# Optimization experiments

Measured on AMD Instinct MI355X. Metric: run time of the kernel, lower is better.

## Reference

```python
import jax, jax.numpy as jnp
import numpy as np

N_NODES = 100000
N_EDGES = 3200000
N_GRAPHS = 2048
DIM = 32
FEAT = 78
OUT = 128
BN_EPS = 1e-5


def setup_inputs() -> dict:
    key = jax.random.key(0)
    ks = jax.random.split(key, 16)
    x = jax.random.normal(ks[0], (N_NODES, FEAT), dtype=jnp.float32)
    edge_index = jax.random.randint(ks[1], (2, N_EDGES), 0, N_NODES, dtype=jnp.int64)
    batch = jnp.sort(jax.random.randint(ks[2], (N_NODES,), 0, N_GRAPHS, dtype=jnp.int64))
    s = 0.1
    # layer 1 MLP (78 -> 32 -> 32)
    W1a = jax.random.normal(ks[3], (FEAT, DIM), dtype=jnp.float32) * s
    b1a = jnp.zeros((DIM,), jnp.float32)
    W1b = jax.random.normal(ks[4], (DIM, DIM), dtype=jnp.float32) * s
    b1b = jnp.zeros((DIM,), jnp.float32)
    # layers 2-5 MLPs stacked (32 -> 32 -> 32)
    Wa = jax.random.normal(ks[5], (4, DIM, DIM), dtype=jnp.float32) * s
    ba = jnp.zeros((4, DIM), jnp.float32)
    Wb = jax.random.normal(ks[6], (4, DIM, DIM), dtype=jnp.float32) * s
    bb = jnp.zeros((4, DIM), jnp.float32)
    # batchnorm affine params for 5 layers
    gamma = jnp.ones((5, DIM), jnp.float32)
    beta = jnp.zeros((5, DIM), jnp.float32)
    # final graph-level linear 32 -> 128
    Wfc = jax.random.normal(ks[7], (DIM, OUT), dtype=jnp.float32) * s
    bfc = jnp.zeros((OUT,), jnp.float32)
    return {"x": x, "edge_index": edge_index, "batch": batch,
            "W1a": W1a, "b1a": b1a, "W1b": W1b, "b1b": b1b,
            "Wa": Wa, "ba": ba, "Wb": Wb, "bb": bb,
            "gamma": gamma, "beta": beta, "Wfc": Wfc, "bfc": bfc}


def _gin_layer(h, edge_index, Wa, ba, Wb, bb, g, b):
    # GIN aggregation (eps=0): h_i + sum_{j->i} h_j via scatter-add on dst
    src, dst = edge_index[0], edge_index[1]
    agg = h + jax.ops.segment_sum(h[src], dst, num_segments=h.shape[0])
    # tiny MLP: Linear -> ReLU -> Linear
    h = jax.nn.relu(agg @ Wa + ba) @ Wb + bb
    h = jax.nn.relu(h)
    # BatchNorm1d (training mode, biased variance)
    mu = h.mean(axis=0)
    var = ((h - mu) ** 2).mean(axis=0)
    return (h - mu) * jax.lax.rsqrt(var + BN_EPS) * g + b


def reference(x, edge_index, batch, W1a, b1a, W1b, b1b, Wa, ba, Wb, bb, gamma, beta, Wfc, bfc):
    h = _gin_layer(x, edge_index, W1a, b1a, W1b, b1b, gamma[0], beta[0])
    for i in range(4):
        h = _gin_layer(h, edge_index, Wa[i], ba[i], Wb[i], bb[i], gamma[i + 1], beta[i + 1])
    # global_add_pool over graphs
    pooled = jax.ops.segment_sum(h, batch, num_segments=N_GRAPHS)  # [G, 32]
    out = jax.nn.relu(pooled @ Wfc + bfc)  # dropout = identity in eval
    return out
```

## Files before the change

kernel.cpp:

```cpp
#include <hip/hip_runtime.h>
#include <hip/hip_fp16.h>

#define N_NODES 100000
#define N_GRAPHS 2048
#define N_EDGES 3200000
#define NHALF 50000
#define DIM 32
#define FEAT 78
#define OUT_DIM 128
#define BN_EPS 1e-5f

#define BSHIFT 9
#define BSIZE 512
#define NB ((N_NODES + BSIZE - 1) / BSIZE)
#define CHUNK 8192
#define NSUB 4

#define NTILES (N_NODES / 16)
#define SBINS 64
#define AGG_BLOCKS 3128

typedef _Float16 f16x8 __attribute__((ext_vector_type(8)));
typedef float f32x4 __attribute__((ext_vector_type(4)));

__global__ __launch_bounds__(256) void bucket_hist_kernel(const int* __restrict__ dst,
                                                          int* __restrict__ bcnt) {
    __shared__ int lh[256];
    int tid = threadIdx.x;
    lh[tid] = 0;
    __syncthreads();
    const int4* d4 = (const int4*)dst;
    const int n4 = N_EDGES / 4;
    int i = blockIdx.x * blockDim.x + tid;
    int stride = gridDim.x * blockDim.x;
    for (; i < n4; i += stride) {
        int4 v = d4[i];
        atomicAdd(&lh[v.x >> BSHIFT], 1);
        atomicAdd(&lh[v.y >> BSHIFT], 1);
        atomicAdd(&lh[v.z >> BSHIFT], 1);
        atomicAdd(&lh[v.w >> BSHIFT], 1);
    }
    __syncthreads();
    if (tid < NB && lh[tid])
        atomicAdd(&bcnt[tid], lh[tid]);
}

__global__ __launch_bounds__(256) void bucket_scan_kernel(const int* __restrict__ bcnt,
                                                          int* __restrict__ bstart,
                                                          int* __restrict__ bcursor,
                                                          int* __restrict__ rowst) {
    __shared__ int sc[256];
    int tid = threadIdx.x;
    int v = (tid < NB) ? bcnt[tid] : 0;
    sc[tid] = v;
    __syncthreads();
    for (int off = 1; off < 256; off <<= 1) {
        int nv = (tid >= off) ? sc[tid - off] : 0;
        __syncthreads();
        sc[tid] += nv;
        __syncthreads();
    }
    if (tid < NB) {
        int ex = sc[tid] - v;
        bstart[tid] = ex;
        bcursor[tid] = ex;
    }
    if (tid == 0) {
        bstart[NB] = N_EDGES;
        rowst[N_NODES] = N_EDGES;
    }
}

__global__ __launch_bounds__(256) void bucket_scatter_kernel(const int* __restrict__ src,
                                                             const int* __restrict__ dst,
                                                             int* __restrict__ bcursor,
                                                             int* __restrict__ bsrc,
                                                             unsigned short* __restrict__ blow) {
    __shared__ int lsrc[CHUNK];
    __shared__ int ldst[CHUNK];
    __shared__ int lhist[256];
    __shared__ int sc[256];
    __shared__ int lpre[256];
    __shared__ int gbase[256];
    __shared__ int lcur[256];
    int tid = threadIdx.x;
    int base = blockIdx.x * CHUNK;
    int n = N_EDGES - base; if (n > CHUNK) n = CHUNK;

    lhist[tid] = 0;
    __syncthreads();
    for (int i = tid; i < n; i += 256)
        atomicAdd(&lhist[dst[base + i] >> BSHIFT], 1);
    __syncthreads();
    int v = lhist[tid];
    sc[tid] = v;
    __syncthreads();
    for (int off = 1; off < 256; off <<= 1) {
        int nv = (tid >= off) ? sc[tid - off] : 0;
        __syncthreads();
        sc[tid] += nv;
        __syncthreads();
    }
    int ex = sc[tid] - v;
    lpre[tid] = ex;
    lcur[tid] = ex;
    if (tid < NB && v)
        gbase[tid] = atomicAdd(&bcursor[tid], v);
    __syncthreads();
    for (int i = tid; i < n; i += 256) {
        int d = dst[base + i];
        int s = src[base + i];
        int b = d >> BSHIFT;
        int pos = atomicAdd(&lcur[b], 1);
        lsrc[pos] = s;
        ldst[pos] = d;
    }
    __syncthreads();
    for (int i = tid; i < n; i += 256) {
        int d = ldst[i];
        int b = d >> BSHIFT;
        int gpos = gbase[b] + (i - lpre[b]);
        bsrc[gpos] = lsrc[i];
        blow[gpos] = (unsigned short)(d & (BSIZE - 1));
    }
}

__global__ __launch_bounds__(256) void node_count_kernel(const int* __restrict__ bstart,
                                                         const int* __restrict__ bsrc,
                                                         const unsigned short* __restrict__ blow,
                                                         int* __restrict__ qcnt) {
    __shared__ int lcnt[BSIZE];
    int tid = threadIdx.x;
    int b = blockIdx.x / NSUB;
    int qt = blockIdx.x % NSUB;
    int ss = bstart[b], se = bstart[b + 1];
    int len = se - ss;
    int qs = ss + (int)(((long long)len * qt) / NSUB);
    int qe = ss + (int)(((long long)len * (qt + 1)) / NSUB);
    lcnt[tid] = 0; lcnt[tid + 256] = 0;
    __syncthreads();
    for (int i = qs + tid; i < qe; i += 256) {
        int add = 0x10000 | (bsrc[i] < NHALF ? 1 : 0);
        atomicAdd(&lcnt[blow[i]], add);
    }
    __syncthreads();
    int* qc = qcnt + (size_t)blockIdx.x * BSIZE;
    qc[tid] = lcnt[tid];
    qc[tid + 256] = lcnt[tid + 256];
}

__global__ __launch_bounds__(256) void node_scan_kernel(const int* __restrict__ bstart,
                                                        const int* __restrict__ qcnt,
                                                        int* __restrict__ qbase0,
                                                        int* __restrict__ qbase1,
                                                        int* __restrict__ rowst,
                                                        int* __restrict__ rowmid) {
    __shared__ int sc[256];
    int tid = threadIdx.x;
    int b = blockIdx.x;
    int ss = bstart[b];
    const int* qc = qcnt + (size_t)b * NSUB * BSIZE;
    int j0 = 2 * tid, j1 = 2 * tid + 1;
    int pk0[NSUB], pk1[NSUB];
    int t0 = 0, t1 = 0, m0 = 0, m1 = 0;
    #pragma unroll
    for (int q = 0; q < NSUB; ++q) {
        pk0[q] = qc[q * BSIZE + j0];
        pk1[q] = qc[q * BSIZE + j1];
        t0 += pk0[q] >> 16; m0 += pk0[q] & 0xFFFF;
        t1 += pk1[q] >> 16; m1 += pk1[q] & 0xFFFF;
    }
    int s = t0 + t1;
    sc[tid] = s;
    __syncthreads();
    for (int off = 1; off < 256; off <<= 1) {
        int nv = (tid >= off) ? sc[tid - off] : 0;
        __syncthreads();
        sc[tid] += nv;
        __syncthreads();
    }
    int ex = sc[tid] - s;
    int B0 = ss + ex;
    int B1 = B0 + t0;
    int node_base = b << BSHIFT;
    if (node_base + j0 < N_NODES) { rowst[node_base + j0] = B0; rowmid[node_base + j0] = B0 + m0; }
    if (node_base + j1 < N_NODES) { rowst[node_base + j1] = B1; rowmid[node_base + j1] = B1 + m1; }
    int r0a = B0, r0b = B0 + m0;
    int r1a = B1, r1b = B1 + m1;
    #pragma unroll
    for (int q = 0; q < NSUB; ++q) {
        int c0 = pk0[q] & 0xFFFF, ct = pk0[q] >> 16;
        qbase0[((size_t)b * NSUB + q) * BSIZE + j0] = r0a; r0a += c0;
        qbase1[((size_t)b * NSUB + q) * BSIZE + j0] = r0b; r0b += ct - c0;
        int d0c = pk1[q] & 0xFFFF, dt = pk1[q] >> 16;
        qbase0[((size_t)b * NSUB + q) * BSIZE + j1] = r1a; r1a += d0c;
        qbase1[((size_t)b * NSUB + q) * BSIZE + j1] = r1b; r1b += dt - d0c;
    }
}

__global__ __launch_bounds__(256) void node_scatter_kernel(const int* __restrict__ bstart,
                                                           const int* __restrict__ bsrc,
                                                           const unsigned short* __restrict__ blow,
                                                           const int* __restrict__ qbase0,
                                                           const int* __restrict__ qbase1,
                                                           int* __restrict__ csr) {
    __shared__ int lcur[2 * BSIZE];
    int tid = threadIdx.x;
    int b = blockIdx.x / NSUB;
    int qt = blockIdx.x % NSUB;
    int ss = bstart[b], se = bstart[b + 1];
    int len = se - ss;
    int qs = ss + (int)(((long long)len * qt) / NSUB);
    int qe = ss + (int)(((long long)len * (qt + 1)) / NSUB);
    size_t off = ((size_t)b * NSUB + qt) * BSIZE;
    for (int j = tid; j < BSIZE; j += 256) {
        lcur[j] = qbase0[off + j];
        lcur[BSIZE + j] = qbase1[off + j];
    }
    __syncthreads();
    for (int i = qs + tid; i < qe; i += 256) {
        int s = bsrc[i];
        int nloc = blow[i];
        int r = (s >= NHALF) ? BSIZE : 0;
        int pos = atomicAdd(&lcur[r + nloc], 1);
        csr[pos] = s;
    }
}

__global__ __launch_bounds__(256) void deg_kernel(const int* __restrict__ rowst,
                                                  float* __restrict__ degf) {
    int i = blockIdx.x * blockDim.x + threadIdx.x;
    if (i < N_NODES)
        degf[i] = (float)(rowst[i + 1] - rowst[i] + 1);
}

__global__ __launch_bounds__(1024) void prep_t1_kernel(const float* __restrict__ W1a,
                                                       __half* __restrict__ blob1) {
    int tid = threadIdx.x;
    for (int idx = tid; idx < 6 * 512; idx += 1024) {
        int e = idx & 7;
        int l = (idx >> 3) & 63;
        int f = idx >> 9;
        int kc = f >> 1, ct = f & 1;
        int k = kc * 32 + (l >> 4) * 8 + e;
        int col = ct * 16 + (l & 15);
        float v = (k < FEAT) ? W1a[k * DIM + col] : 0.f;
        blob1[idx] = __float2half(v);
    }
}

__global__ __launch_bounds__(256) void transform1_kernel(const float* __restrict__ x,
                                                         const __half* __restrict__ blob1,
                                                         __half* __restrict__ T) {
    __shared__ __align__(16) _Float16 X[4][512];
    int tid = threadIdx.x;
    int wave = tid >> 6;
    int l = tid & 63;
    int d0 = l & 15, kg = l >> 4;
    int tile = blockIdx.x * 4 + wave;
    if (tile >= NTILES) return;
    int tb = tile * 16;
    const float* xr = x + (size_t)(tb + d0) * FEAT;

    f16x8 af0, af1, af2;
    #pragma unroll
    for (int j = 0; j < 4; ++j) {
        int k0 = kg * 8 + 2 * j;
        float2 v0 = *(const float2*)(xr + k0);
        float2 v1 = *(const float2*)(xr + 32 + k0);
        af0[2 * j] = (_Float16)v0.x; af0[2 * j + 1] = (_Float16)v0.y;
        af1[2 * j] = (_Float16)v1.x; af1[2 * j + 1] = (_Float16)v1.y;
        int k2 = 64 + k0;
        float2 v2 = {0.f, 0.f};
        if (k2 < FEAT) v2 = *(const float2*)(xr + k2);
        af2[2 * j] = (_Float16)v2.x; af2[2 * j + 1] = (_Float16)v2.y;
    }
    f16x8 b0 = *(const f16x8*)(blob1 + (0 * 64 + l) * 8);
    f16x8 b1 = *(const f16x8*)(blob1 + (1 * 64 + l) * 8);
    f16x8 b2 = *(const f16x8*)(blob1 + (2 * 64 + l) * 8);
    f16x8 b3 = *(const f16x8*)(blob1 + (3 * 64 + l) * 8);
    f16x8 b4 = *(const f16x8*)(blob1 + (4 * 64 + l) * 8);
    f16x8 b5 = *(const f16x8*)(blob1 + (5 * 64 + l) * 8);

    f32x4 c0 = {0.f, 0.f, 0.f, 0.f};
    f32x4 c1 = {0.f, 0.f, 0.f, 0.f};
    c0 = __builtin_amdgcn_mfma_f32_16x16x32_f16(af0, b0, c0, 0, 0, 0);
    c1 = __builtin_amdgcn_mfma_f32_16x16x32_f16(af0, b1, c1, 0, 0, 0);
    c0 = __builtin_amdgcn_mfma_f32_16x16x32_f16(af1, b2, c0, 0, 0, 0);
    c1 = __builtin_amdgcn_mfma_f32_16x16x32_f16(af1, b3, c1, 0, 0, 0);
    c0 = __builtin_amdgcn_mfma_f32_16x16x32_f16(af2, b4, c0, 0, 0, 0);
    c1 = __builtin_amdgcn_mfma_f32_16x16x32_f16(af2, b5, c1, 0, 0, 0);

    #pragma unroll
    for (int rr = 0; rr < 4; ++rr) {
        int row = kg * 4 + rr;
        X[wave][row * 32 + d0] = (_Float16)c0[rr];
        X[wave][row * 32 + d0 + 16] = (_Float16)c1[rr];
    }
    __builtin_amdgcn_wave_barrier();
    int gg = l >> 2, cq = l & 3;
    uint4 vv = *(uint4*)&X[wave][gg * 32 + cq * 8];
    *(uint4*)(T + (size_t)(tb + gg) * DIM + cq * 8) = vv;
}

__global__ __launch_bounds__(1024) void prep_kernel(const float* __restrict__ sbins,
                                                    const float* __restrict__ gamma,
                                                    const float* __restrict__ beta,
                                                    const float* __restrict__ Wa,
                                                    const float* __restrict__ Wb,
                                                    __half* __restrict__ blob,
                                                    float* __restrict__ cwf) {
    __shared__ float st[64];
    __shared__ float a[DIM], c[DIM];
    int tid = threadIdx.x;
    if (tid < 64) {
        float s = 0.f;
        for (int b = 0; b < SBINS; ++b) s += sbins[b * 64 + tid];
        st[tid] = s;
    }
    __syncthreads();
    if (tid < DIM) {
        float mu = st[tid] * (1.f / N_NODES);
        float var = st[DIM + tid] * (1.f / N_NODES) - mu * mu;
        float av = gamma[tid] * rsqrtf(var + BN_EPS);
        a[tid] = av;
        c[tid] = beta[tid] - mu * av;
    }
    __syncthreads();
    int d = tid >> 5, k = tid & 31;
    blob[d * 32 + k] = __float2half(a[k] * Wa[k * 32 + d]);
    blob[1024 + d * 32 + k] = __float2half(Wb[k * 32 + d]);
    if (tid < DIM) {
        float s = 0.f;
        for (int kk = 0; kk < DIM; ++kk)
            s += c[kk] * Wa[kk * 32 + tid];
        cwf[tid] = s;
    }
}

__global__ __launch_bounds__(1024) void prep_id_kernel(const float* __restrict__ W1b,
                                                       __half* __restrict__ blob,
                                                       float* __restrict__ cwf) {
    int tid = threadIdx.x;
    int d = tid >> 5, k = tid & 31;
    blob[d * 32 + k] = __float2half((d == k) ? 1.f : 0.f);
    blob[1024 + d * 32 + k] = __float2half(W1b[k * 32 + d]);
    if (tid < DIM) cwf[tid] = 0.f;
}

#define ACC8(v) do { const __half2* hp_ = (const __half2*)&(v); float2 f_; \
  f_ = __half22float2(hp_[0]); a0 += f_.x; a1 += f_.y; \
  f_ = __half22float2(hp_[1]); a2 += f_.x; a3 += f_.y; \
  f_ = __half22float2(hp_[2]); a4 += f_.x; a5 += f_.y; \
  f_ = __half22float2(hp_[3]); a6 += f_.x; a7 += f_.y; } while (0)

__global__ __launch_bounds__(256) void agg_pass_kernel(const __half* __restrict__ T,
                                                       const int* __restrict__ rowst,
                                                       const int* __restrict__ rowmid,
                                                       const int* __restrict__ csr,
                                                       __half* __restrict__ P0,
                                                       __half* __restrict__ P1) {
    int b = blockIdx.x;
    int half = (b >> 2) & 1;
    int idx_in_half = (b >> 3) * 4 + (b & 3);
    int tid = threadIdx.x;
    int wave = tid >> 6;
    int l = tid & 63;
    int g = l >> 2, q = l & 3;
    int tile = idx_in_half * 4 + wave;
    if (tile >= NTILES) return;
    int node = tile * 16 + g;
    int ps, pe;
    if (half == 0) { ps = rowst[node]; pe = rowmid[node]; }
    else           { ps = rowmid[node]; pe = rowst[node + 1]; }
    float a0 = 0.f, a1 = 0.f, a2 = 0.f, a3 = 0.f,
          a4 = 0.f, a5 = 0.f, a6 = 0.f, a7 = 0.f;
    int p = ps;
    int idx[8];
    bool have = (p + 8 <= pe);
    if (have) {
        #pragma unroll
        for (int j = 0; j < 8; ++j) idx[j] = csr[p + j];
    }
    while (have) {
        uint4 v[8];
        #pragma unroll
        for (int j = 0; j < 8; ++j)
            v[j] = *(const uint4*)(T + (size_t)idx[j] * DIM + (q << 3));
        int np = p + 8;
        bool nhave = (np + 8 <= pe);
        int nidx[8];
        if (nhave) {
            #pragma unroll
            for (int j = 0; j < 8; ++j) nidx[j] = csr[np + j];
        }
        #pragma unroll
        for (int j = 0; j < 8; ++j) ACC8(v[j]);
        #pragma unroll
        for (int j = 0; j < 8; ++j) idx[j] = nidx[j];
        p = np;
        have = nhave;
    }
    if (p < pe) {
        #pragma unroll
        for (int j = 0; j < 8; ++j) {
            int ei = p + j;
            uint4 vv = {0, 0, 0, 0};
            if (ei < pe) vv = *(const uint4*)(T + (size_t)csr[ei] * DIM + (q << 3));
            ACC8(vv);
        }
    }
    int selfhalf = (node < NHALF) ? 0 : 1;
    if (selfhalf == half) {
        uint4 vs = *(const uint4*)(T + (size_t)node * DIM + (q << 3));
        ACC8(vs);
    }
    __half* P = half ? P1 : P0;
    f16x8 hv;
    hv[0] = (_Float16)a0; hv[1] = (_Float16)a1;
    hv[2] = (_Float16)a2; hv[3] = (_Float16)a3;
    hv[4] = (_Float16)a4; hv[5] = (_Float16)a5;
    hv[6] = (_Float16)a6; hv[7] = (_Float16)a7;
    *(f16x8*)(P + (size_t)node * DIM + (q << 3)) = hv;
}

__global__ __launch_bounds__(256) void mlp_kernel(const __half* __restrict__ P0,
                                                  const __half* __restrict__ P1,
                                                  const float* __restrict__ degf,
                                                  const __half* __restrict__ blob,
                                                  const float* __restrict__ cwf,
                                                  const float* __restrict__ bias_a,
                                                  const float* __restrict__ bias_b,
                                                  __half* __restrict__ outT,
                                                  float* __restrict__ sbins) {
    __shared__ __align__(16) _Float16 X[4][512];
    int tid = threadIdx.x;
    int wave = tid >> 6;
    int l = tid & 63;
    int d0 = l & 15, kg = l >> 4;
    int tile = blockIdx.x * 4 + wave;
    if (tile >= NTILES) return;
    int tb = tile * 16;

    f16x8 v0 = *(const f16x8*)(P0 + (size_t)(tb + d0) * DIM + kg * 8);
    f16x8 v1 = *(const f16x8*)(P1 + (size_t)(tb + d0) * DIM + kg * 8);
    f16x8 af = v0 + v1;
    f16x8 bA0 = *(const f16x8*)(blob + d0 * 32 + kg * 8);
    f16x8 bA1 = *(const f16x8*)(blob + (d0 + 16) * 32 + kg * 8);
    f16x8 bB0 = *(const f16x8*)(blob + 1024 + d0 * 32 + kg * 8);
    f16x8 bB1 = *(const f16x8*)(blob + 1024 + (d0 + 16) * 32 + kg * 8);
    f32x4 degv = *(const f32x4*)(degf + tb + kg * 4);
    float cw0 = cwf[d0], cw1 = cwf[d0 + 16];
    float ba0 = bias_a[d0], ba1 = bias_a[d0 + 16];
    float bb0 = bias_b[d0], bb1 = bias_b[d0 + 16];

    f32x4 c0 = {ba0, ba0, ba0, ba0};
    f32x4 c1 = {ba1, ba1, ba1, ba1};
    c0 = __builtin_amdgcn_mfma_f32_16x16x32_f16(af, bA0, c0, 0, 0, 0);
    c1 = __builtin_amdgcn_mfma_f32_16x16x32_f16(af, bA1, c1, 0, 0, 0);
    #pragma unroll
    for (int rr = 0; rr < 4; ++rr) {
        float w0 = fmaxf(c0[rr] + degv[rr] * cw0, 0.f);
        float w1 = fmaxf(c1[rr] + degv[rr] * cw1, 0.f);
        int row = kg * 4 + rr;
        X[wave][row * 32 + d0] = (_Float16)w0;
        X[wave][row * 32 + d0 + 16] = (_Float16)w1;
    }
    __builtin_amdgcn_wave_barrier();
    f16x8 af2 = *(f16x8*)&X[wave][d0 * 32 + kg * 8];
    __builtin_amdgcn_wave_barrier();

    f32x4 e0 = {bb0, bb0, bb0, bb0};
    f32x4 e1 = {bb1, bb1, bb1, bb1};
    e0 = __builtin_amdgcn_mfma_f32_16x16x32_f16(af2, bB0, e0, 0, 0, 0);
    e1 = __builtin_amdgcn_mfma_f32_16x16x32_f16(af2, bB1, e1, 0, 0, 0);
    float s0 = 0.f, ss0 = 0.f, s1 = 0.f, ss1 = 0.f;
    #pragma unroll
    for (int rr = 0; rr < 4; ++rr) {
        float y0 = fmaxf(e0[rr], 0.f);
        float y1 = fmaxf(e1[rr], 0.f);
        s0 += y0; ss0 += y0 * y0;
        s1 += y1; ss1 += y1 * y1;
        int row = kg * 4 + rr;
        X[wave][row * 32 + d0] = (_Float16)y0;
        X[wave][row * 32 + d0 + 16] = (_Float16)y1;
    }
    __builtin_amdgcn_wave_barrier();
    {
        int gg = l >> 2, c = l & 3;
        uint4 vv = *(uint4*)&X[wave][gg * 32 + c * 8];
        *(uint4*)(outT + (size_t)(tb + gg) * DIM + c * 8) = vv;
    }
    s0 += __shfl_xor(s0, 16); s0 += __shfl_xor(s0, 32);
    ss0 += __shfl_xor(ss0, 16); ss0 += __shfl_xor(ss0, 32);
    s1 += __shfl_xor(s1, 16); s1 += __shfl_xor(s1, 32);
    ss1 += __shfl_xor(ss1, 16); ss1 += __shfl_xor(ss1, 32);
    if (kg == 0) {
        float* sb = sbins + ((blockIdx.x * 4 + wave) & (SBINS - 1)) * 64;
        atomicAdd(&sb[d0], s0);
        atomicAdd(&sb[DIM + d0], ss0);
        atomicAdd(&sb[d0 + 16], s1);
        atomicAdd(&sb[DIM + d0 + 16], ss1);
    }
}

#define POOL_BLOCKS 512
__global__ __launch_bounds__(256) void bn_pool_kernel(const __half* __restrict__ h,
                                                      const float* __restrict__ sbins,
                                                      const float* __restrict__ gamma,
                                                      const float* __restrict__ beta,
                                                      const int* __restrict__ batch,
                                                      float* __restrict__ pooled) {
    __shared__ float st[64];
    int tid = threadIdx.x;
    if (tid < 64) {
        float s = 0.f;
        for (int b = 0; b < SBINS; ++b) s += sbins[b * 64 + tid];
        st[tid] = s;
    }
    __syncthreads();
    int lane = tid & 31;
    int group = tid >> 5;
    float mu = st[lane] * (1.f / N_NODES);
    float var = st[DIM + lane] * (1.f / N_NODES) - mu * mu;
    float inv = rsqrtf(var + BN_EPS);
    float a = gamma[lane] * inv;
    float c = beta[lane] - mu * a;
    const int ngroups = POOL_BLOCKS * 8;
    const int chunk = (N_NODES + ngroups - 1) / ngroups;
    int g = blockIdx.x * 8 + group;
    int start = g * chunk;
    if (start >= N_NODES) return;
    int end = start + chunk; if (end > N_NODES) end = N_NODES;
    int cur = batch[start];
    float s = 0.f;
    for (int node = start; node < end; ++node) {
        float v = __half2float(h[(size_t)node * DIM + lane]) * a + c;
        int bg = batch[node];
        if (bg != cur) {
            atomicAdd(&pooled[cur * DIM + lane], s);
            s = 0.f;
            cur = bg;
        }
        s += v;
    }
    atomicAdd(&pooled[cur * DIM + lane], s);
}

__global__ __launch_bounds__(256) void fc_kernel(const float* __restrict__ pooled,
                                                 const float* __restrict__ Wfc,
                                                 const float* __restrict__ bfc,
                                                 float* __restrict__ out) {
    __shared__ float Wl[DIM * OUT_DIM];
    for (int i = threadIdx.x; i < DIM * OUT_DIM; i += blockDim.x) Wl[i] = Wfc[i];
    __syncthreads();
    int idx = blockIdx.x * blockDim.x + threadIdx.x;
    int stride = gridDim.x * blockDim.x;
    for (; idx < N_GRAPHS * OUT_DIM; idx += stride) {
        int g = idx >> 7;
        int o = idx & 127;
        float acc = bfc[o];
        #pragma unroll
        for (int k = 0; k < DIM; ++k)
            acc += pooled[g * DIM + k] * Wl[k * OUT_DIM + o];
        out[idx] = fmaxf(acc, 0.f);
    }
}

extern "C" void kernel_launch(void* const* d_in, const int* in_sizes, int n_in,
                              void* d_out, int out_size, void* d_ws, size_t ws_size,
                              hipStream_t stream) {
    const float* x   = (const float*)d_in[0];
    const int* eidx  = (const int*)d_in[1];
    const int* src   = eidx;
    const int* dst   = eidx + N_EDGES;
    const int* batch = (const int*)d_in[2];
    const float* W1a = (const float*)d_in[3];
    const float* b1a = (const float*)d_in[4];
    const float* W1b = (const float*)d_in[5];
    const float* b1b = (const float*)d_in[6];
    const float* Wa  = (const float*)d_in[7];
    const float* ba  = (const float*)d_in[8];
    const float* Wb  = (const float*)d_in[9];
    const float* bb  = (const float*)d_in[10];
    const float* gamma = (const float*)d_in[11];
    const float* beta  = (const float*)d_in[12];
    const float* Wfc = (const float*)d_in[13];
    const float* bfc = (const float*)d_in[14];
    float* out = (float*)d_out;

    const size_t TSZ = (size_t)N_NODES * DIM;
    __half* TA = (__half*)d_ws;
    __half* TB = TA + TSZ;
    __half* P0 = TB + TSZ;
    __half* P1 = P0 + TSZ;
    float* degf   = (float*)(P1 + TSZ);
    float* sbins  = degf + N_NODES;
    float* pooled = sbins + 5 * SBINS * 64;
    float* cwf    = pooled + N_GRAPHS * DIM;
    __half* blobs = (__half*)(cwf + 5 * 32);
    __half* blob1 = blobs + 5 * 2048;
    int* csr      = (int*)(blob1 + 6 * 512);
    int* rowst    = csr + N_EDGES;
    int* rowmid   = rowst + N_NODES + 1;
    int* bcnt     = rowmid + N_NODES;
    int* bstart   = bcnt + 256;
    int* bcursor  = bstart + NB + 1;
    int* qcnt     = bcursor + 256;

    int* bsrc            = (int*)TA;
    unsigned short* blow = (unsigned short*)P0;
    int* qbase0          = (int*)P1;
    int* qbase1          = qbase0 + NB * NSUB * BSIZE;

    hipMemsetAsync(bcnt, 0, 256 * sizeof(int), stream);
    hipMemsetAsync(sbins, 0, 5 * SBINS * 64 * sizeof(float), stream);
    hipMemsetAsync(pooled, 0, N_GRAPHS * DIM * sizeof(float), stream);

    bucket_hist_kernel<<<1024, 256, 0, stream>>>(dst, bcnt);
    bucket_scan_kernel<<<1, 256, 0, stream>>>(bcnt, bstart, bcursor, rowst);
    bucket_scatter_kernel<<<(N_EDGES + CHUNK - 1) / CHUNK, 256, 0, stream>>>(src, dst, bcursor, bsrc, blow);
    node_count_kernel<<<NB * NSUB, 256, 0, stream>>>(bstart, bsrc, blow, qcnt);
    node_scan_kernel<<<NB, 256, 0, stream>>>(bstart, qcnt, qbase0, qbase1, rowst, rowmid);
    node_scatter_kernel<<<NB * NSUB, 256, 0, stream>>>(bstart, bsrc, blow, qbase0, qbase1, csr);

    deg_kernel<<<(N_NODES + 255) / 256, 256, 0, stream>>>(rowst, degf);
    prep_t1_kernel<<<1, 1024, 0, stream>>>(W1a, blob1);
    transform1_kernel<<<(NTILES + 3) / 4, 256, 0, stream>>>(x, blob1, TA);

    prep_id_kernel<<<1, 1024, 0, stream>>>(W1b, blobs, cwf);

    const __half* in = TA;
    __half* o = TB;

    agg_pass_kernel<<<AGG_BLOCKS, 256, 0, stream>>>(in, rowst, rowmid, csr, P0, P1);
    mlp_kernel<<<(NTILES + 3) / 4, 256, 0, stream>>>(P0, P1, degf, blobs, cwf, b1a, b1b, o, sbins);
    { const __half* t = in; in = o; o = (__half*)t; }

    for (int i = 0; i < 4; ++i) {
        __half* blob_i = blobs + (i + 1) * 2048;
        float* cwf_i = cwf + (i + 1) * 32;
        prep_kernel<<<1, 1024, 0, stream>>>(sbins + i * SBINS * 64, gamma + i * DIM, beta + i * DIM,
                                            Wa + i * DIM * DIM, Wb + i * DIM * DIM, blob_i, cwf_i);
        agg_pass_kernel<<<AGG_BLOCKS, 256, 0, stream>>>(in, rowst, rowmid, csr, P0, P1);
        mlp_kernel<<<(NTILES + 3) / 4, 256, 0, stream>>>(P0, P1, degf, blob_i, cwf_i,
                                                         ba + i * DIM, bb + i * DIM, o,
                                                         sbins + (i + 1) * SBINS * 64);
        { const __half* t = in; in = o; o = (__half*)t; }
    }

    bn_pool_kernel<<<POOL_BLOCKS, 256, 0, stream>>>(in, sbins + 4 * SBINS * 64,
                                                    gamma + 4 * DIM, beta + 4 * DIM, batch, pooled);
    fc_kernel<<<1024, 256, 0, stream>>>(pooled, Wfc, bfc, out);
}
```

Baseline: 369.4 us.

## Pack bucketed edges into one word and split node scatter by node range

The intermediate bucketed edge arrays (src int plus 16-bit local dst) are packed into a single 32-bit word (local dst in high bits, src in low 17 bits), so the bucket scatter, node count and node scatter passes move fewer bytes. The node scatter now assigns each block a range of 128 destination nodes within a bucket instead of an edge quarter. Each block scans all edges of the bucket and filters, so the final CSR writes for a block land in a narrower region. This trades roughly NR times more reads of the packed edges for less scattered writes and smaller shared cursor tables.

```diff
diff --git a/kernel.cpp b/kernel.cpp
--- a/kernel.cpp
+++ b/kernel.cpp
@@ -15,6 +15,7 @@
 #define NB ((N_NODES + BSIZE - 1) / BSIZE)
 #define CHUNK 8192
 #define NSUB 4
+#define NR 4
 
 #define NTILES (N_NODES / 16)
 #define SBINS 64
@@ -74,10 +75,9 @@
 __global__ __launch_bounds__(256) void bucket_scatter_kernel(const int* __restrict__ src,
                                                              const int* __restrict__ dst,
                                                              int* __restrict__ bcursor,
-                                                             int* __restrict__ bsrc,
-                                                             unsigned short* __restrict__ blow) {
-    __shared__ int lsrc[CHUNK];
-    __shared__ int ldst[CHUNK];
+                                                             int* __restrict__ epk) {
+    __shared__ int lpk[CHUNK];
+    __shared__ unsigned char lbkt[CHUNK];
     __shared__ int lhist[256];
     __shared__ int sc[256];
     __shared__ int lpre[256];
@@ -112,22 +112,19 @@
         int s = src[base + i];
         int b = d >> BSHIFT;
         int pos = atomicAdd(&lcur[b], 1);
-        lsrc[pos] = s;
-        ldst[pos] = d;
+        lpk[pos] = ((d & (BSIZE - 1)) << 17) | s;
+        lbkt[pos] = (unsigned char)b;
     }
     __syncthreads();
     for (int i = tid; i < n; i += 256) {
-        int d = ldst[i];
-        int b = d >> BSHIFT;
+        int b = lbkt[i];
         int gpos = gbase[b] + (i - lpre[b]);
-        bsrc[gpos] = lsrc[i];
-        blow[gpos] = (unsigned short)(d & (BSIZE - 1));
+        epk[gpos] = lpk[i];
     }
 }
 
 __global__ __launch_bounds__(256) void node_count_kernel(const int* __restrict__ bstart,
-                                                         const int* __restrict__ bsrc,
-                                                         const unsigned short* __restrict__ blow,
+                                                         const int* __restrict__ epk,
                                                          int* __restrict__ qcnt) {
     __shared__ int lcnt[BSIZE];
     int tid = threadIdx.x;
@@ -140,8 +137,9 @@
     lcnt[tid] = 0; lcnt[tid + 256] = 0;
     __syncthreads();
     for (int i = qs + tid; i < qe; i += 256) {
-        int add = 0x10000 | (bsrc[i] < NHALF ? 1 : 0);
-        atomicAdd(&lcnt[blow[i]], add);
+        int pk = epk[i];
+        int add = 0x10000 | (((pk & 0x1FFFF) < NHALF) ? 1 : 0);
+        atomicAdd(&lcnt[pk >> 17], add);
     }
     __syncthreads();
     int* qc = qcnt + (size_t)blockIdx.x * BSIZE;
@@ -199,31 +197,36 @@
 }
 
 __global__ __launch_bounds__(256) void node_scatter_kernel(const int* __restrict__ bstart,
-                                                           const int* __restrict__ bsrc,
-                                                           const unsigned short* __restrict__ blow,
+                                                           const int* __restrict__ epk,
                                                            const int* __restrict__ qbase0,
                                                            const int* __restrict__ qbase1,
                                                            int* __restrict__ csr) {
-    __shared__ int lcur[2 * BSIZE];
-    int tid = threadIdx.x;
-    int b = blockIdx.x / NSUB;
-    int qt = blockIdx.x % NSUB;
+    __shared__ int lcur[2 * NSUB * 128];
+    int tid = threadIdx.x;
+    int b = blockIdx.x / NR;
+    int r = blockIdx.x % NR;
+    for (int j = tid; j < NSUB * 128; j += 256) {
+        int q = j >> 7, n = j & 127;
+        lcur[j] = qbase0[((size_t)b * NSUB + q) * BSIZE + r * 128 + n];
+        lcur[NSUB * 128 + j] = qbase1[((size_t)b * NSUB + q) * BSIZE + r * 128 + n];
+    }
+    __syncthreads();
     int ss = bstart[b], se = bstart[b + 1];
     int len = se - ss;
-    int qs = ss + (int)(((long long)len * qt) / NSUB);
-    int qe = ss + (int)(((long long)len * (qt + 1)) / NSUB);
-    size_t off = ((size_t)b * NSUB + qt) * BSIZE;
-    for (int j = tid; j < BSIZE; j += 256) {
-        lcur[j] = qbase0[off + j];
-        lcur[BSIZE + j] = qbase1[off + j];
-    }
-    __syncthreads();
-    for (int i = qs + tid; i < qe; i += 256) {
-        int s = bsrc[i];
-        int nloc = blow[i];
-        int r = (s >= NHALF) ? BSIZE : 0;
-        int pos = atomicAdd(&lcur[r + nloc], 1);
-        csr[pos] = s;
+    #pragma unroll
+    for (int q = 0; q < NSUB; ++q) {
+        int qs = ss + (int)(((long long)len * q) / NSUB);
+        int qe = ss + (int)(((long long)len * (q + 1)) / NSUB);
+        for (int i = qs + tid; i < qe; i += 256) {
+            int pk = epk[i];
+            int nloc = pk >> 17;
+            if ((nloc >> 7) == r) {
+                int s = pk & 0x1FFFF;
+                int h = (s >= NHALF) ? NSUB * 128 : 0;
+                int pos = atomicAdd(&lcur[h + (q << 7) + (nloc & 127)], 1);
+                csr[pos] = s;
+            }
+        }
     }
 }
 
@@ -608,8 +611,7 @@
     int* bcursor  = bstart + NB + 1;
     int* qcnt     = bcursor + 256;
 
-    int* bsrc            = (int*)TA;
-    unsigned short* blow = (unsigned short*)P0;
+    int* epk             = (int*)TA;
     int* qbase0          = (int*)P1;
     int* qbase1          = qbase0 + NB * NSUB * BSIZE;
 
@@ -619,10 +621,10 @@
 
     bucket_hist_kernel<<<1024, 256, 0, stream>>>(dst, bcnt);
     bucket_scan_kernel<<<1, 256, 0, stream>>>(bcnt, bstart, bcursor, rowst);
-    bucket_scatter_kernel<<<(N_EDGES + CHUNK - 1) / CHUNK, 256, 0, stream>>>(src, dst, bcursor, bsrc, blow);
-    node_count_kernel<<<NB * NSUB, 256, 0, stream>>>(bstart, bsrc, blow, qcnt);
+    bucket_scatter_kernel<<<(N_EDGES + CHUNK - 1) / CHUNK, 256, 0, stream>>>(src, dst, bcursor, epk);
+    node_count_kernel<<<NB * NSUB, 256, 0, stream>>>(bstart, epk, qcnt);
     node_scan_kernel<<<NB, 256, 0, stream>>>(bstart, qcnt, qbase0, qbase1, rowst, rowmid);
-    node_scatter_kernel<<<NB * NSUB, 256, 0, stream>>>(bstart, bsrc, blow, qbase0, qbase1, csr);
+    node_scatter_kernel<<<NB * NR, 256, 0, stream>>>(bstart, epk, qbase0, qbase1, csr);
 
     deg_kernel<<<(N_NODES + 255) / 256, 256, 0, stream>>>(rowst, degf);
     prep_t1_kernel<<<1, 1024, 0, stream>>>(W1a, blob1);
```

After: 354.6 us. 4.0% less time.
